# Performance work log

Hardware: AMD Instinct MI355X
Metric: run time of the kernel (lower is better)

## Reference

```python
import jax, jax.numpy as jnp
import numpy as np
from jax import lax

BN_EPS = 1e-5
HEADS = 2


def dw_conv(x, w, stride, pad):
    # depthwise conv, NCHW, weight OIHW with I=1, groups=C
    return lax.conv_general_dilated(
        x, w, (stride, stride), [(pad, pad), (pad, pad)],
        dimension_numbers=('NCHW', 'OIHW', 'NCHW'),
        feature_group_count=x.shape[1])


def bn(x, g, b, m, v):
    inv = g * lax.rsqrt(v + BN_EPS)
    return (x - m[:, None, None]) * inv[:, None, None] + b[:, None, None]


def conv1x1(x, w, b):
    return jnp.einsum('bchw,oc->bohw', x, w) + b[:, None, None]


def setup_inputs() -> dict:
    key = jax.random.key(0)
    ks = jax.random.split(key, 20)
    B, C, H, W = 32, 128, 56, 56
    r = lambda i, shape, s=0.05: jax.random.normal(ks[i], shape, jnp.float32) * s
    return {
        'x': jax.random.normal(ks[0], (B, C, H, W), jnp.float32),
        'q_w': r(1, (C, C)), 'q_b': r(2, (C,)),
        'kv_w': r(3, (2 * C, C)), 'kv_b': r(4, (2 * C,)),
        'sr1_w': r(5, (C, 1, 4, 4), 0.2),
        'sr1_g': jax.random.uniform(ks[6], (C,), jnp.float32) + 0.5,
        'sr1_b': r(7, (C,)),
        'sr1_m': r(8, (C,)),
        'sr1_v': jax.random.uniform(ks[9], (C,), jnp.float32) + 0.5,
        'sr2_w': r(10, (C, 1, 1, 1), 0.5),
        'sr2_g': jax.random.uniform(ks[11], (C,), jnp.float32) + 0.5,
        'sr2_b': r(12, (C,)),
        'sr2_m': r(13, (C,)),
        'sr2_v': jax.random.uniform(ks[14], (C,), jnp.float32) + 0.5,
        'local_w': r(15, (C, 1, 3, 3), 0.2), 'local_b': r(16, (C,)),
    }


def reference(x, q_w, q_b, kv_w, kv_b,
              sr1_w, sr1_g, sr1_b, sr1_m, sr1_v,
              sr2_w, sr2_g, sr2_b, sr2_m, sr2_v,
              local_w, local_b):
    B, C, H, W = x.shape
    h = HEADS
    d = C // h
    scale = d ** -0.5

    # q projection: 1x1 conv -> [B, h, N, d]
    q = conv1x1(x, q_w, q_b)
    q = q.reshape(B, h, d, H * W).transpose(0, 1, 3, 2)

    # spatial reduction: depthwise strided conv + BN + ReLU, then depthwise 1x1 + BN
    kv = jax.nn.relu(bn(dw_conv(x, sr1_w, 4, 2), sr1_g, sr1_b, sr1_m, sr1_v))
    kv = bn(kv * sr2_w.reshape(C, 1, 1), sr2_g, sr2_b, sr2_m, sr2_v)

    # depthwise 3x3 local conv + residual
    kv = dw_conv(kv, local_w, 1, 1) + local_b[:, None, None] + kv

    # kv projection and split
    kvp = conv1x1(kv, kv_w, kv_b)
    k, v = jnp.split(kvp, 2, axis=1)
    Nk = k.shape[2] * k.shape[3]
    k = k.reshape(B, h, d, Nk)                       # [B,h,d,Nk]
    v = v.reshape(B, h, d, Nk).transpose(0, 1, 3, 2)  # [B,h,Nk,d]

    attn = jax.nn.softmax(jnp.einsum('bhnd,bhdm->bhnm', q, k) * scale, axis=-1)
    out = jnp.einsum('bhnm,bhmd->bhnd', attn, v)      # [B,h,N,d]
    return out.transpose(0, 1, 3, 2).reshape(B, C, H, W)
```

## Files before the change

### kernel.cpp

```cpp
#include <hip/hip_runtime.h>
#include <hip/hip_bf16.h>

#define B_    32
#define C_    128
#define H_    56
#define W_    56
#define N_    3136
#define HK_   15
#define NK_   225
#define D_    64

typedef __attribute__((ext_vector_type(8))) short bf16x8;
typedef __attribute__((ext_vector_type(4))) float f32x4;

__device__ __forceinline__ float b2f(unsigned short u) {
    union { float f; unsigned int i; } x;
    x.i = ((unsigned int)u) << 16;
    return x.f;
}
__device__ __forceinline__ unsigned short f2b(float f) {
    __hip_bfloat16 h = __float2bfloat16(f);
    return *(unsigned short*)&h;
}

__device__ __forceinline__ void gll16(const char* g, char* l) {
    __builtin_amdgcn_global_load_lds(
        (const __attribute__((address_space(1))) unsigned int*)g,
        (__attribute__((address_space(3))) unsigned int*)l,
        16, 0, 0);
}

__global__ __launch_bounds__(256) void srlocal_kernel(
        const float* __restrict__ x,
        const float* __restrict__ sr1_w, const float* __restrict__ sr1_g,
        const float* __restrict__ sr1_b, const float* __restrict__ sr1_m,
        const float* __restrict__ sr1_v, const float* __restrict__ sr2_w,
        const float* __restrict__ sr2_g, const float* __restrict__ sr2_b,
        const float* __restrict__ sr2_m, const float* __restrict__ sr2_v,
        const float* __restrict__ local_w, const float* __restrict__ local_b,
        float* __restrict__ kv2) {
    int bc = blockIdx.x;
    int c  = bc & (C_ - 1);
    int tid = threadIdx.x;
    __shared__ float xim[H_ * W_];
    __shared__ float kvt[HK_][HK_ + 1];

    const float* xp = x + (size_t)bc * (H_ * W_);
    for (int idx = tid; idx < (H_ * W_) / 4; idx += 256)
        ((float4*)xim)[idx] = ((const float4*)xp)[idx];
    __syncthreads();

    int p = tid;
    int oy = p / HK_, ox = p % HK_;
    if (p < NK_) {
        float s = 0.f;
#pragma unroll
        for (int ky = 0; ky < 4; ++ky) {
            int iy = oy * 4 - 2 + ky;
            if (iy < 0 || iy >= H_) continue;
#pragma unroll
            for (int kx = 0; kx < 4; ++kx) {
                int ix = ox * 4 - 2 + kx;
                if (ix < 0 || ix >= W_) continue;
                s += xim[iy * W_ + ix] * sr1_w[c * 16 + ky * 4 + kx];
            }
        }
        float inv1 = sr1_g[c] * rsqrtf(sr1_v[c] + 1e-5f);
        s = (s - sr1_m[c]) * inv1 + sr1_b[c];
        s = fmaxf(s, 0.f);
        s *= sr2_w[c];
        float inv2 = sr2_g[c] * rsqrtf(sr2_v[c] + 1e-5f);
        s = (s - sr2_m[c]) * inv2 + sr2_b[c];
        kvt[oy][ox] = s;
    }
    __syncthreads();
    if (p < NK_) {
        float v = kvt[oy][ox] + local_b[c];
#pragma unroll
        for (int dy = -1; dy <= 1; ++dy) {
            int yy = oy + dy;
            if (yy < 0 || yy >= HK_) continue;
#pragma unroll
            for (int dx = -1; dx <= 1; ++dx) {
                int xx = ox + dx;
                if (xx < 0 || xx >= HK_) continue;
                v += kvt[yy][xx] * local_w[c * 9 + (dy + 1) * 3 + (dx + 1)];
            }
        }
        kv2[(size_t)bc * NK_ + p] = v;
    }
}

__global__ __launch_bounds__(256) void wprep_kernel(
        const float* __restrict__ q_w, const float* __restrict__ q_b,
        const float* __restrict__ kv_w, const float* __restrict__ kv_b,
        unsigned short* __restrict__ wkq_sw, unsigned short* __restrict__ wv_sw,
        float* __restrict__ kwb, float* __restrict__ wb, float* __restrict__ qkb) {
    int bx = blockIdx.x;
    int h  = bx >> 3, cg = bx & 7;
    int tid = threadIdx.x;
    __shared__ float wk_s[64][128];
    __shared__ float wq_s[64][16];

    for (int idx = tid; idx < 64 * 128; idx += 256)
        wk_s[idx >> 7][idx & 127] = kv_w[(size_t)(h * 64 + (idx >> 7)) * 128 + (idx & 127)];
    for (int idx = tid; idx < 64 * 16; idx += 256)
        wq_s[idx >> 4][idx & 15] = q_w[(size_t)(h * 64 + (idx >> 4)) * 128 + cg * 16 + (idx & 15)];
    __syncthreads();

    {
        int cl = tid >> 4;
        int c  = cg * 16 + cl;
        int cp0 = (tid & 15) * 8;
        float acc[8];
#pragma unroll
        for (int i = 0; i < 8; ++i) acc[i] = 0.f;
        for (int e = 0; e < 64; ++e) {
            float wqv = wq_s[e][cl];
#pragma unroll
            for (int i = 0; i < 8; ++i) acc[i] += wqv * wk_s[e][cp0 + i];
        }
        char* base = (char*)wkq_sw + (size_t)h * 32768 + (size_t)c * 256;
        ushort4 u0, u1;
        u0.x = f2b(acc[0] * 0.125f); u0.y = f2b(acc[1] * 0.125f);
        u0.z = f2b(acc[2] * 0.125f); u0.w = f2b(acc[3] * 0.125f);
        u1.x = f2b(acc[4] * 0.125f); u1.y = f2b(acc[5] * 0.125f);
        u1.z = f2b(acc[6] * 0.125f); u1.w = f2b(acc[7] * 0.125f);
        int sw = (c & 7) << 4;
        *(ushort4*)(base + ((cp0 * 2) ^ sw)) = u0;
        *(ushort4*)(base + ((cp0 * 2 + 8) ^ sw)) = u1;
    }
    if (tid < 16) {
        int cl = tid, c = cg * 16 + cl;
        float s = 0.f;
        for (int e = 0; e < 64; ++e) s += kv_b[h * 64 + e] * wq_s[e][cl];
        kwb[h * 128 + c] = s * 0.125f;
    }
    if (cg == 0) {
        if (tid < 128) {
            float s = 0.f;
            for (int e = 0; e < 64; ++e) s += q_b[h * 64 + e] * wk_s[e][tid];
            wb[h * 128 + tid] = s * 0.125f;
        }
        if (tid == 0) {
            float s = 0.f;
            for (int e = 0; e < 64; ++e) s += q_b[h * 64 + e] * kv_b[h * 64 + e];
            qkb[h] = s * 0.125f;
        }
    }
    if (cg == 1) {
        for (int idx = tid; idx < 64 * 128; idx += 256) {
            int e = idx >> 7, cp = idx & 127;
            unsigned short val = f2b(kv_w[(size_t)(128 + h * 64 + e) * 128 + cp]);
            *(unsigned short*)((char*)wv_sw + (size_t)h * 16384 + (size_t)e * 256 +
                               (((cp * 2) ^ ((e & 7) << 4)))) = val;
        }
    }
}

#define L2B(r, cb) ((r) * 256 + ((cb) ^ (((r) & 7) << 4)))
__global__ __launch_bounds__(256, 2) void kvw_kernel(
        const float* __restrict__ kv2,
        const float* __restrict__ kv_b,
        const unsigned short* __restrict__ wkq_sw,
        const unsigned short* __restrict__ wv_sw,
        const float* __restrict__ kwb,
        const float* __restrict__ wb,
        const float* __restrict__ qkb,
        unsigned short* __restrict__ kw,
        float* __restrict__ bias_s,
        unsigned short* __restrict__ vbuf) {
    int b = blockIdx.x, h = blockIdx.y, mh = blockIdx.z;
    int bh = b * 2 + h;
    int m0 = mh * 64;
    int tid = threadIdx.x;
    int lo = tid & 15, hi = (tid >> 4) & 3, wid = tid >> 6;

    __shared__ char K2[16384];
    __shared__ char WQ[32768];
    __shared__ char WV[16384];

    {
        const char* srcQ = (const char*)wkq_sw + (size_t)h * 32768 + tid * 16;
        char* dstQ = WQ + wid * 1024;
#pragma unroll
        for (int i = 0; i < 8; ++i) gll16(srcQ + i * 4096, dstQ + i * 4096);
        const char* srcV = (const char*)wv_sw + (size_t)h * 16384 + tid * 16;
        char* dstV = WV + wid * 1024;
#pragma unroll
        for (int i = 0; i < 4; ++i) gll16(srcV + i * 4096, dstV + i * 4096);
    }
    {
        int j = tid & 63;
        int mg = m0 + j;
        bool val = (mg < NK_);
#pragma unroll
        for (int it = 0; it < 8; ++it) {
            int c0 = (tid >> 6) * 4 + it * 16;
            ushort4 u;
            if (val) {
                const float* kp = kv2 + ((size_t)b * 128 + c0) * NK_ + mg;
                u.x = f2b(kp[0]);
                u.y = f2b(kp[NK_]);
                u.z = f2b(kp[2 * NK_]);
                u.w = f2b(kp[3 * NK_]);
            } else { u.x = 0; u.y = 0; u.z = 0; u.w = 0; }
            *(ushort4*)(K2 + L2B(j, c0 * 2)) = u;
        }
    }
    __syncthreads();

    bf16x8 aq[4];
#pragma unroll
    for (int ks = 0; ks < 4; ++ks)
        aq[ks] = *(const bf16x8*)(K2 + L2B(wid * 16 + lo, ks * 64 + hi * 16));

    char* kwB = (char*)kw + (size_t)bh * 65536;
#pragma unroll
    for (int ct = 0; ct < 8; ++ct) {
        f32x4 acc = {0.f, 0.f, 0.f, 0.f};
#pragma unroll
        for (int ks = 0; ks < 4; ++ks) {
            bf16x8 bq = *(const bf16x8*)(WQ + L2B(ct * 16 + lo, ks * 64 + hi * 16));
            acc = __builtin_amdgcn_mfma_f32_16x16x32_bf16(aq[ks], bq, acc, 0, 0, 0);
        }
        int c = ct * 16 + lo;
        float kb = kwb[h * 128 + c];
#pragma unroll
        for (int r = 0; r < 4; ++r) {
            int mg = m0 + wid * 16 + hi * 4 + r;
            *(unsigned short*)(kwB + (size_t)mg * 256 + (((c * 2) ^ ((mg & 7) << 4)))) =
                f2b(acc[r] + kb);
        }
    }

    char* vB = (char*)vbuf + (size_t)bh * 32768;
#pragma unroll
    for (int et = 0; et < 4; ++et) {
        f32x4 acc = {0.f, 0.f, 0.f, 0.f};
#pragma unroll
        for (int ks = 0; ks < 4; ++ks) {
            bf16x8 bv = *(const bf16x8*)(WV + L2B(et * 16 + lo, ks * 64 + hi * 16));
            acc = __builtin_amdgcn_mfma_f32_16x16x32_bf16(aq[ks], bv, acc, 0, 0, 0);
        }
        int e = et * 16 + lo;
        float vb = kv_b[128 + h * 64 + e];
#pragma unroll
        for (int r = 0; r < 4; ++r) {
            int mg = m0 + wid * 16 + hi * 4 + r;
            *(unsigned short*)(vB + (size_t)e * 512 + (((mg * 2) ^ ((e & 7) << 4)))) =
                f2b(acc[r] + vb);
        }
    }

    if (tid < 64) {
        int mg = m0 + tid;
        float s;
        if (mg >= NK_) s = -1e30f;
        else {
            s = qkb[h];
            for (int i = 0; i < 128; ++i) {
                int cp = (i + (tid & 7) * 16) & 127;
                s += b2f(*(const unsigned short*)(K2 + L2B(tid, cp * 2))) * wb[h * 128 + cp];
            }
        }
        bias_s[(size_t)bh * 256 + mg] = s;
    }
}

#define XTB(j, c) ((j) * 256 + (((c) * 2) ^ (((j) & 15) << 4)))
#define PSB(j, m) ((j) * 512 + (((m) * 2) ^ (((j) & 15) << 4)))
#define KWB(rl, cb) ((rl) * 256 + ((cb) ^ (((rl) & 7) << 4)))
#define CVB(e, cb)  ((e) * 512 + ((cb) ^ (((e) & 7) << 4)))

__global__ __launch_bounds__(256, 2) void attn_kernel(
        const float* __restrict__ x,
        const unsigned short* __restrict__ kw,
        const float* __restrict__ bias_s,
        const unsigned short* __restrict__ vbuf,
        float* __restrict__ out) {
    int jt = blockIdx.x;
    int h  = blockIdx.y;
    int bb = blockIdx.z;
    int n0 = jt * 64;
    int bh = bb * 2 + h;
    int tid = threadIdx.x;
    int lo  = tid & 15;
    int hi  = (tid >> 4) & 3;
    int wid = tid >> 6;
    int jw  = wid * 16;

    __shared__ char A[32768];
    __shared__ char Bt[2][8192];
    __shared__ char Cv[32768];

    const char* kwG = (const char*)kw + (size_t)bh * 65536;
    const char* vG  = (const char*)vbuf + (size_t)bh * 32768;

#pragma unroll
    for (int it = 0; it < 8; ++it) {
        int j  = tid & 63;
        int c0 = (tid >> 6) * 4 + it * 16;
        const float* xp = x + ((size_t)bb * 128 + c0) * N_ + n0 + j;
        ushort4 u;
        u.x = f2b(xp[0]);
        u.y = f2b(xp[(size_t)N_]);
        u.z = f2b(xp[2 * (size_t)N_]);
        u.w = f2b(xp[3 * (size_t)N_]);
        *(ushort4*)(A + XTB(j, c0)) = u;
    }
    {
        float bsl = bias_s[(size_t)bh * 256 + tid];
        *(float*)(A + 16384 + tid * 4) = bsl;
    }
    {
        const char* s0 = kwG + tid * 16;
        char* d0 = Bt[0] + wid * 1024;
        gll16(s0, d0); gll16(s0 + 4096, d0 + 4096);
        const char* s1 = kwG + 8192 + tid * 16;
        char* d1 = Bt[1] + wid * 1024;
        gll16(s1, d1); gll16(s1 + 4096, d1 + 4096);
        const char* sc = vG + tid * 16;
        char* dc = Cv + wid * 1024;
#pragma unroll
        for (int i = 0; i < 8; ++i) gll16(sc + i * 4096, dc + i * 4096);
    }
    asm volatile("s_waitcnt vmcnt(10) lgkmcnt(0)" ::: "memory");
    __builtin_amdgcn_s_barrier();
    __builtin_amdgcn_sched_barrier(0);

    bf16x8 aq[4];
#pragma unroll
    for (int ks = 0; ks < 4; ++ks)
        aq[ks] = *(const bf16x8*)(A + XTB(jw + lo, ks * 32 + hi * 8));

    f32x4 s[16];
#pragma unroll
    for (int t = 0; t < 8; ++t) {
#pragma unroll
        for (int ml = 0; ml < 2; ++ml) {
            f32x4 acc = {0.f, 0.f, 0.f, 0.f};
#pragma unroll
            for (int ks = 0; ks < 4; ++ks) {
                bf16x8 bk = *(const bf16x8*)(Bt[t & 1] + KWB(ml * 16 + lo, ks * 64 + hi * 16));
                acc = __builtin_amdgcn_mfma_f32_16x16x32_bf16(aq[ks], bk, acc, 0, 0, 0);
            }
            s[t * 2 + ml] = acc;
        }
        if (t < 6) {
            __builtin_amdgcn_s_barrier();
            const char* sn = kwG + (t + 2) * 8192 + tid * 16;
            char* dn = Bt[t & 1] + wid * 1024;
            gll16(sn, dn); gll16(sn + 4096, dn + 4096);
        }
        if (t < 7) {
            if (t == 0)      asm volatile("s_waitcnt vmcnt(10)" ::: "memory");
            else if (t < 6)  asm volatile("s_waitcnt vmcnt(2)" ::: "memory");
            else             asm volatile("s_waitcnt vmcnt(0)" ::: "memory");
            __builtin_amdgcn_s_barrier();
            __builtin_amdgcn_sched_barrier(0);
        }
    }

    float bs[16];
#pragma unroll
    for (int mt = 0; mt < 16; ++mt)
        bs[mt] = *(const float*)(A + 16384 + (mt * 16 + lo) * 4);
#pragma unroll
    for (int mt = 0; mt < 16; ++mt) {
#pragma unroll
        for (int r = 0; r < 4; ++r) s[mt][r] += bs[mt];
    }
    asm volatile("s_waitcnt lgkmcnt(0)" ::: "memory");
    __builtin_amdgcn_s_barrier();
    __builtin_amdgcn_sched_barrier(0);

    float mx[4];
#pragma unroll
    for (int r = 0; r < 4; ++r) {
        float m0v = s[0][r];
#pragma unroll
        for (int mt = 1; mt < 16; ++mt) m0v = fmaxf(m0v, s[mt][r]);
        mx[r] = m0v;
    }
#pragma unroll
    for (int d = 1; d < 16; d <<= 1) {
#pragma unroll
        for (int r = 0; r < 4; ++r) mx[r] = fmaxf(mx[r], __shfl_xor(mx[r], d));
    }
    float sm[4] = {0.f, 0.f, 0.f, 0.f};
#pragma unroll
    for (int mt = 0; mt < 16; ++mt) {
#pragma unroll
        for (int r = 0; r < 4; ++r) {
            float pe = __expf(s[mt][r] - mx[r]);
            s[mt][r] = pe;
            sm[r] += pe;
        }
    }
#pragma unroll
    for (int d = 1; d < 16; d <<= 1) {
#pragma unroll
        for (int r = 0; r < 4; ++r) sm[r] += __shfl_xor(sm[r], d);
    }
    float rinv[4];
#pragma unroll
    for (int r = 0; r < 4; ++r) rinv[r] = 1.f / sm[r];

#pragma unroll
    for (int mt = 0; mt < 16; ++mt) {
#pragma unroll
        for (int r = 0; r < 4; ++r)
            *(unsigned short*)(A + PSB(jw + hi * 4 + r, mt * 16 + lo)) =
                f2b(s[mt][r] * rinv[r]);
    }

    bf16x8 bp[8];
#pragma unroll
    for (int ks = 0; ks < 8; ++ks)
        bp[ks] = *(const bf16x8*)(A + PSB(jw + lo, ks * 32 + hi * 8));
#pragma unroll
    for (int et = 0; et < 4; ++et) {
        f32x4 acc = {0.f, 0.f, 0.f, 0.f};
#pragma unroll
        for (int ks = 0; ks < 8; ++ks) {
            bf16x8 av = *(const bf16x8*)(Cv + CVB(et * 16 + lo, ks * 64 + hi * 16));
            acc = __builtin_amdgcn_mfma_f32_16x16x32_bf16(av, bp[ks], acc, 0, 0, 0);
        }
        int e = et * 16 + hi * 4;
#pragma unroll
        for (int r = 0; r < 4; ++r)
            out[((size_t)bb * 128 + h * 64 + e + r) * N_ + n0 + jw + lo] = acc[r];
    }
}

extern "C" void kernel_launch(void* const* d_in, const int* in_sizes, int n_in,
                              void* d_out, int out_size, void* d_ws, size_t ws_size,
                              hipStream_t stream) {
    const float* x       = (const float*)d_in[0];
    const float* q_w     = (const float*)d_in[1];
    const float* q_b     = (const float*)d_in[2];
    const float* kv_w    = (const float*)d_in[3];
    const float* kv_b    = (const float*)d_in[4];
    const float* sr1_w   = (const float*)d_in[5];
    const float* sr1_g   = (const float*)d_in[6];
    const float* sr1_b   = (const float*)d_in[7];
    const float* sr1_m   = (const float*)d_in[8];
    const float* sr1_v   = (const float*)d_in[9];
    const float* sr2_w   = (const float*)d_in[10];
    const float* sr2_g   = (const float*)d_in[11];
    const float* sr2_b   = (const float*)d_in[12];
    const float* sr2_m   = (const float*)d_in[13];
    const float* sr2_v   = (const float*)d_in[14];
    const float* local_w = (const float*)d_in[15];
    const float* local_b = (const float*)d_in[16];

    char* ws = (char*)d_ws;
    float* kv2              = (float*)(ws + 0);
    unsigned short* wkq_sw  = (unsigned short*)(ws + 3686400);
    unsigned short* wv_sw   = (unsigned short*)(ws + 3751936);
    unsigned short* kw      = (unsigned short*)(ws + 3784704);
    unsigned short* vbuf    = (unsigned short*)(ws + 7979008);
    float* bias_s           = (float*)(ws + 10076160);
    float* kwb              = (float*)(ws + 10141696);
    float* wb               = (float*)(ws + 10142720);
    float* qkb              = (float*)(ws + 10143744);

    wprep_kernel<<<16, 256, 0, stream>>>(q_w, q_b, kv_w, kv_b,
                                         wkq_sw, wv_sw, kwb, wb, qkb);
    srlocal_kernel<<<B_ * C_, 256, 0, stream>>>(
        x, sr1_w, sr1_g, sr1_b, sr1_m, sr1_v,
        sr2_w, sr2_g, sr2_b, sr2_m, sr2_v, local_w, local_b, kv2);
    kvw_kernel<<<dim3(B_, 2, 4), 256, 0, stream>>>(
        kv2, kv_b, wkq_sw, wv_sw, kwb, wb, qkb, kw, bias_s, vbuf);
    attn_kernel<<<dim3(49, 2, B_), 256, 0, stream>>>(
        x, kw, bias_s, vbuf, (float*)d_out);
}
```

Before: 105.9 us.

## Drop V LDS staging, load V from global into registers, raise attn occupancy

The V tile is no longer staged in a 32KB shared buffer. Each wave now loads its V fragments straight from global memory into registers and interleaves those loads with the PV MFMAs. The score bias goes to registers instead of LDS, and launch bounds rise to 3 blocks per SM. The grid is flattened and remapped so blocks for the same batch-head land on the same XCD for L2 reuse. In exchange there are more register-resident V fragments and uncoalesced or redundant global V reads across waves, which may add register pressure under the tighter launch bound.

```diff
diff --git a/kernel.cpp b/kernel.cpp
--- a/kernel.cpp
+++ b/kernel.cpp
@@ -234,7 +234,7 @@
         }
     }
 
-    char* vB = (char*)vbuf + (size_t)bh * 32768;
+    unsigned short* vB = vbuf + (size_t)bh * 64 * 256;
 #pragma unroll
     for (int et = 0; et < 4; ++et) {
         f32x4 acc = {0.f, 0.f, 0.f, 0.f};
@@ -248,8 +248,7 @@
 #pragma unroll
         for (int r = 0; r < 4; ++r) {
             int mg = m0 + wid * 16 + hi * 4 + r;
-            *(unsigned short*)(vB + (size_t)e * 512 + (((mg * 2) ^ ((e & 7) << 4)))) =
-                f2b(acc[r] + vb);
+            vB[e * 256 + mg] = f2b(acc[r] + vb);
         }
     }
 
@@ -271,19 +270,40 @@
 #define XTB(j, c) ((j) * 256 + (((c) * 2) ^ (((j) & 15) << 4)))
 #define PSB(j, m) ((j) * 512 + (((m) * 2) ^ (((j) & 15) << 4)))
 #define KWB(rl, cb) ((rl) * 256 + ((cb) ^ (((rl) & 7) << 4)))
-#define CVB(e, cb)  ((e) * 512 + ((cb) ^ (((e) & 7) << 4)))
-
-__global__ __launch_bounds__(256, 2) void attn_kernel(
+
+#define LOADV(dst, ET) do {                                                        \
+    _Pragma("unroll")                                                              \
+    for (int ks = 0; ks < 8; ++ks)                                                 \
+        dst[ks] = *(const bf16x8*)(vG + (size_t)((ET) * 16 + lo) * 256 +           \
+                                   ks * 32 + hi * 8);                              \
+} while (0)
+
+#define PVET(ET, avr) do {                                                         \
+    f32x4 acc = {0.f, 0.f, 0.f, 0.f};                                              \
+    _Pragma("unroll")                                                              \
+    for (int ks = 0; ks < 8; ++ks)                                                 \
+        acc = __builtin_amdgcn_mfma_f32_16x16x32_bf16(avr[ks], bp[ks], acc, 0, 0, 0); \
+    int e = (ET) * 16 + hi * 4;                                                    \
+    _Pragma("unroll")                                                              \
+    for (int r = 0; r < 4; ++r)                                                    \
+        out[((size_t)bb * 128 + h * 64 + e + r) * N_ + n0 + jw + lo] = acc[r];     \
+} while (0)
+
+__global__ __launch_bounds__(256, 3) void attn_kernel(
         const float* __restrict__ x,
         const unsigned short* __restrict__ kw,
         const float* __restrict__ bias_s,
         const unsigned short* __restrict__ vbuf,
         float* __restrict__ out) {
-    int jt = blockIdx.x;
-    int h  = blockIdx.y;
-    int bb = blockIdx.z;
-    int n0 = jt * 64;
-    int bh = bb * 2 + h;
+    int flat = blockIdx.x;
+    int xcd  = flat & 7;
+    int idx  = flat >> 3;
+    int g    = idx / 49;
+    int jt   = idx % 49;
+    int bh   = g * 8 + xcd;
+    int bb   = bh >> 1;
+    int h    = bh & 1;
+    int n0   = jt * 64;
     int tid = threadIdx.x;
     int lo  = tid & 15;
     int hi  = (tid >> 4) & 3;
@@ -292,10 +312,24 @@
 
     __shared__ char A[32768];
     __shared__ char Bt[2][8192];
-    __shared__ char Cv[32768];
 
     const char* kwG = (const char*)kw + (size_t)bh * 65536;
-    const char* vG  = (const char*)vbuf + (size_t)bh * 32768;
+    const unsigned short* vG = vbuf + (size_t)bh * 64 * 256;
+
+    {
+        const char* s0 = kwG + tid * 16;
+        char* d0 = Bt[0] + wid * 1024;
+        gll16(s0, d0); gll16(s0 + 4096, d0 + 4096);
+        const char* s1 = kwG + 8192 + tid * 16;
+        char* d1 = Bt[1] + wid * 1024;
+        gll16(s1, d1); gll16(s1 + 4096, d1 + 4096);
+    }
+    __builtin_amdgcn_sched_barrier(0);
+
+    float bs[16];
+    const float* bsp = bias_s + (size_t)bh * 256;
+#pragma unroll
+    for (int mt = 0; mt < 16; ++mt) bs[mt] = bsp[mt * 16 + lo];
 
 #pragma unroll
     for (int it = 0; it < 8; ++it) {
@@ -309,25 +343,7 @@
         u.w = f2b(xp[3 * (size_t)N_]);
         *(ushort4*)(A + XTB(j, c0)) = u;
     }
-    {
-        float bsl = bias_s[(size_t)bh * 256 + tid];
-        *(float*)(A + 16384 + tid * 4) = bsl;
-    }
-    {
-        const char* s0 = kwG + tid * 16;
-        char* d0 = Bt[0] + wid * 1024;
-        gll16(s0, d0); gll16(s0 + 4096, d0 + 4096);
-        const char* s1 = kwG + 8192 + tid * 16;
-        char* d1 = Bt[1] + wid * 1024;
-        gll16(s1, d1); gll16(s1 + 4096, d1 + 4096);
-        const char* sc = vG + tid * 16;
-        char* dc = Cv + wid * 1024;
-#pragma unroll
-        for (int i = 0; i < 8; ++i) gll16(sc + i * 4096, dc + i * 4096);
-    }
-    asm volatile("s_waitcnt vmcnt(10) lgkmcnt(0)" ::: "memory");
-    __builtin_amdgcn_s_barrier();
-    __builtin_amdgcn_sched_barrier(0);
+    __syncthreads();
 
     bf16x8 aq[4];
 #pragma unroll
@@ -354,27 +370,18 @@
             gll16(sn, dn); gll16(sn + 4096, dn + 4096);
         }
         if (t < 7) {
-            if (t == 0)      asm volatile("s_waitcnt vmcnt(10)" ::: "memory");
-            else if (t < 6)  asm volatile("s_waitcnt vmcnt(2)" ::: "memory");
-            else             asm volatile("s_waitcnt vmcnt(0)" ::: "memory");
+            if (t < 5) asm volatile("s_waitcnt vmcnt(2)" ::: "memory");
+            else       asm volatile("s_waitcnt vmcnt(0)" ::: "memory");
             __builtin_amdgcn_s_barrier();
             __builtin_amdgcn_sched_barrier(0);
         }
     }
 
-    float bs[16];
-#pragma unroll
-    for (int mt = 0; mt < 16; ++mt)
-        bs[mt] = *(const float*)(A + 16384 + (mt * 16 + lo) * 4);
 #pragma unroll
     for (int mt = 0; mt < 16; ++mt) {
 #pragma unroll
         for (int r = 0; r < 4; ++r) s[mt][r] += bs[mt];
     }
-    asm volatile("s_waitcnt lgkmcnt(0)" ::: "memory");
-    __builtin_amdgcn_s_barrier();
-    __builtin_amdgcn_sched_barrier(0);
-
     float mx[4];
 #pragma unroll
     for (int r = 0; r < 4; ++r) {
@@ -415,23 +422,19 @@
                 f2b(s[mt][r] * rinv[r]);
     }
 
+    bf16x8 av0[8], av1[8], av2[8], av3[8];
+    LOADV(av0, 0);
+    LOADV(av1, 1);
     bf16x8 bp[8];
 #pragma unroll
     for (int ks = 0; ks < 8; ++ks)
         bp[ks] = *(const bf16x8*)(A + PSB(jw + lo, ks * 32 + hi * 8));
-#pragma unroll
-    for (int et = 0; et < 4; ++et) {
-        f32x4 acc = {0.f, 0.f, 0.f, 0.f};
-#pragma unroll
-        for (int ks = 0; ks < 8; ++ks) {
-            bf16x8 av = *(const bf16x8*)(Cv + CVB(et * 16 + lo, ks * 64 + hi * 16));
-            acc = __builtin_amdgcn_mfma_f32_16x16x32_bf16(av, bp[ks], acc, 0, 0, 0);
-        }
-        int e = et * 16 + hi * 4;
-#pragma unroll
-        for (int r = 0; r < 4; ++r)
-            out[((size_t)bb * 128 + h * 64 + e + r) * N_ + n0 + jw + lo] = acc[r];
-    }
+    PVET(0, av0);
+    LOADV(av2, 2);
+    PVET(1, av1);
+    LOADV(av3, 3);
+    PVET(2, av2);
+    PVET(3, av3);
 }
 
 extern "C" void kernel_launch(void* const* d_in, const int* in_sizes, int n_in,
@@ -473,6 +476,6 @@
         sr2_w, sr2_g, sr2_b, sr2_m, sr2_v, local_w, local_b, kv2);
     kvw_kernel<<<dim3(B_, 2, 4), 256, 0, stream>>>(
         kv2, kv_b, wkq_sw, wv_sw, kwb, wb, qkb, kw, bias_s, vbuf);
-    attn_kernel<<<dim3(49, 2, B_), 256, 0, stream>>>(
+    attn_kernel<<<3136, 256, 0, stream>>>(
         x, kw, bias_s, vbuf, (float*)d_out);
 }
```

After: 131.7 us. +24.4%, slower.
